# Performance work log

Hardware: AMD Instinct MI355X
Metric: run time of the kernel (lower is better)

The kernel has to match this reference:

```python
import jax, jax.numpy as jnp
import numpy as np

N, E, DIM, HEADS = 100000, 800000, 128, 4
CH = DIM // HEADS


def setup_inputs() -> dict:
    key = jax.random.key(0)
    ks = jax.random.split(key, 20)
    s = 0.02
    inp = {
        "x": jax.random.normal(ks[0], (N, DIM), jnp.float32),
        "edge_index": jax.random.randint(ks[1], (2, E), 0, N, jnp.int64 if jax.config.jax_enable_x64 else jnp.int32),
        "edge_attr": jax.random.normal(ks[2], (E, DIM), jnp.float32),
        # per-layer (leading dim 2) TransformerConv params
        "Wq": jax.random.normal(ks[3], (2, DIM, DIM), jnp.float32) * s,
        "bq": jnp.zeros((2, DIM), jnp.float32),
        "Wk": jax.random.normal(ks[4], (2, DIM, DIM), jnp.float32) * s,
        "bk": jnp.zeros((2, DIM), jnp.float32),
        "Wv": jax.random.normal(ks[5], (2, DIM, DIM), jnp.float32) * s,
        "bv": jnp.zeros((2, DIM), jnp.float32),
        "We": jax.random.normal(ks[6], (2, DIM, DIM), jnp.float32) * s,      # lin_edge, no bias
        "Ws": jax.random.normal(ks[7], (2, DIM, DIM), jnp.float32) * s,      # lin_skip
        "bs": jnp.zeros((2, DIM), jnp.float32),
        "Wb": jax.random.normal(ks[8], (2, 3 * DIM, 1), jnp.float32) * s,    # lin_beta, no bias
        "ln_g": jnp.ones((2, DIM), jnp.float32),
        "ln_b": jnp.zeros((2, DIM), jnp.float32),
        "Wo": jax.random.normal(ks[9], (DIM, DIM), jnp.float32) * s,
        "bo": jnp.zeros((DIM,), jnp.float32),
        "Wg": jax.random.normal(ks[10], (DIM, 1), jnp.float32) * s,
        "bg": jnp.zeros((1,), jnp.float32),
    }
    return inp


def _layer_norm(x, g, b, eps=1e-5):
    mu = jnp.mean(x, -1, keepdims=True)
    var = jnp.mean(jnp.square(x - mu), -1, keepdims=True)
    return (x - mu) * jax.lax.rsqrt(var + eps) * g + b


def _tconv(x, src, dst, edge_attr, Wq, bq, Wk, bk, Wv, bv, We, Ws, bs, Wb):
    # TransformerConv (PyG), beta=True, concat=True, eval mode (no dropout)
    q = (x @ Wq + bq).reshape(N, HEADS, CH)
    k = (x @ Wk + bk).reshape(N, HEADS, CH)
    v = (x @ Wv + bv).reshape(N, HEADS, CH)
    e = (edge_attr @ We).reshape(E, HEADS, CH)
    kj = k[src] + e                                    # [E,H,C]
    vj = v[src] + e
    logits = jnp.sum(q[dst] * kj, -1) / np.sqrt(CH)    # [E,H]
    m = jax.ops.segment_max(logits, dst, num_segments=N)
    p = jnp.exp(logits - m[dst])
    denom = jax.ops.segment_sum(p, dst, num_segments=N)
    alpha = p / (denom[dst] + 1e-16)                   # scatter-softmax over in-edges
    msg = (alpha[..., None] * vj).reshape(E, DIM)
    out = jax.ops.segment_sum(msg, dst, num_segments=N)  # [N,DIM]
    x_r = x @ Ws + bs
    beta = jax.nn.sigmoid(jnp.concatenate([out, x_r, out - x_r], -1) @ Wb)  # [N,1]
    return beta * x_r + (1.0 - beta) * out


def reference(x, edge_index, edge_attr, Wq, bq, Wk, bk, Wv, bv, We, Ws, bs, Wb,
              ln_g, ln_b, Wo, bo, Wg, bg):
    src, dst = edge_index[0], edge_index[1]
    gelu = lambda t: jax.nn.gelu(t, approximate=False)
    h = _layer_norm(gelu(_tconv(x, src, dst, edge_attr, Wq[0], bq[0], Wk[0], bk[0],
                                Wv[0], bv[0], We[0], Ws[0], bs[0], Wb[0])), ln_g[0], ln_b[0])
    h2 = _layer_norm(gelu(_tconv(h, src, dst, edge_attr, Wq[1], bq[1], Wk[1], bk[1],
                                 Wv[1], bv[1], We[1], Ws[1], bs[1], Wb[1])), ln_g[1], ln_b[1])
    h = h + h2
    out = h @ Wo + bo
    g = jax.nn.sigmoid(x @ Wg + bg)
    return g * x + (1.0 - g) * out
```

## Files before the change

kernel.cpp:

```cpp
#include <hip/hip_runtime.h>
#include <math.h>

#define NN 100000
#define NE 800000

typedef __attribute__((ext_vector_type(8))) short short8;
typedef __attribute__((ext_vector_type(4))) float f32x4;

__device__ __forceinline__ float bf2f(unsigned short u) {
  union { float f; unsigned int i; } x; x.i = ((unsigned int)u) << 16; return x.f;
}
__device__ __forceinline__ unsigned short f2bf(float f) {
  union { float f; unsigned int i; } x; x.f = f;
  unsigned int r = x.i + 0x7fffu + ((x.i >> 16) & 1u);
  return (unsigned short)(r >> 16);
}

__device__ __forceinline__ short8 load8_f32_as_bf16(const float* p) {
  const float4 a = *(const float4*)p;
  const float4 b = *(const float4*)(p + 4);
  short8 r;
  r[0] = (short)f2bf(a.x); r[1] = (short)f2bf(a.y); r[2] = (short)f2bf(a.z); r[3] = (short)f2bf(a.w);
  r[4] = (short)f2bf(b.x); r[5] = (short)f2bf(b.y); r[6] = (short)f2bf(b.z); r[7] = (short)f2bf(b.w);
  return r;
}

__global__ __launch_bounds__(256) void hist_k(const int* __restrict__ ei, int* __restrict__ deg) {
  int t = blockIdx.x * 256 + threadIdx.x;
  if (t < NE) atomicAdd(&deg[ei[NE + t]], 1);
}

__global__ __launch_bounds__(256) void scan1(const int* __restrict__ deg, int* __restrict__ bsum) {
  __shared__ int sd[256];
  const int b = blockIdx.x, t = threadIdx.x, base = b * 1024;
  int s = 0;
  #pragma unroll
  for (int i = 0; i < 4; i++) { int idx = base + t * 4 + i; if (idx < NN) s += deg[idx]; }
  sd[t] = s; __syncthreads();
  for (int off = 128; off >= 1; off >>= 1) { if (t < off) sd[t] += sd[t + off]; __syncthreads(); }
  if (t == 0) bsum[b] = sd[0];
}

__global__ __launch_bounds__(64) void scan2(int* __restrict__ bsum, int nb, int* __restrict__ rowstart) {
  const int lane = threadIdx.x;
  int v0 = (2 * lane     < nb) ? bsum[2 * lane]     : 0;
  int v1 = (2 * lane + 1 < nb) ? bsum[2 * lane + 1] : 0;
  const int s = v0 + v1;
  int inc = s;
  #pragma unroll
  for (int off = 1; off < 64; off <<= 1) {
    int o = __shfl_up(inc, off, 64);
    if (lane >= off) inc += o;
  }
  const int excl = inc - s;
  if (2 * lane     < nb) bsum[2 * lane]     = excl;
  if (2 * lane + 1 < nb) bsum[2 * lane + 1] = excl + v0;
  if (lane == 63) rowstart[NN] = inc;
}

__global__ __launch_bounds__(256) void scan3(const int* __restrict__ deg, const int* __restrict__ bsum,
                                             int* __restrict__ rowstart, int* __restrict__ cursor) {
  __shared__ int sd[256];
  const int b = blockIdx.x, t = threadIdx.x, base = b * 1024;
  int vals[4]; int s = 0;
  #pragma unroll
  for (int i = 0; i < 4; i++) { int idx = base + t * 4 + i; vals[i] = (idx < NN) ? deg[idx] : 0; s += vals[i]; }
  sd[t] = s; __syncthreads();
  for (int off = 1; off < 256; off <<= 1) {
    int add = (t >= off) ? sd[t - off] : 0;
    __syncthreads();
    sd[t] += add;
    __syncthreads();
  }
  const int excl = sd[t] - s;
  int run = bsum[b] + excl;
  #pragma unroll
  for (int i = 0; i < 4; i++) {
    int idx = base + t * 4 + i;
    if (idx < NN) { rowstart[idx] = run; cursor[idx] = run; run += vals[i]; }
  }
}

__global__ __launch_bounds__(256) void scatter_k(const int* __restrict__ ei, int* __restrict__ cursor,
                                                 int2* __restrict__ rec) {
  int t = blockIdx.x * 256 + threadIdx.x;
  if (t >= NE) return;
  int dst = ei[NE + t];
  int pos = atomicAdd(&cursor[dst], 1);
  rec[pos] = make_int2(ei[t], t);
}

__global__ __launch_bounds__(256) void conv_w(
    const float* __restrict__ Wq, const float* __restrict__ Wk, const float* __restrict__ Wv,
    const float* __restrict__ Ws, const float* __restrict__ We, const float* __restrict__ Wo,
    unsigned short* __restrict__ wT)
{
  int idx = blockIdx.x * 256 + threadIdx.x;
  int m = idx >> 14;
  int r = idx & 16383;
  int n = r >> 7, kk = r & 127;
  const float* src;
  switch (m) {
    case 0: src = Wq; break;
    case 1: src = Wk; break;
    case 2: src = Wv; break;
    case 3: src = Ws; break;
    case 4: src = Wq + 16384; break;
    case 5: src = Wk + 16384; break;
    case 6: src = Wv + 16384; break;
    case 7: src = Ws + 16384; break;
    case 8: src = We; break;
    case 9: src = We + 16384; break;
    default: src = Wo; break;
  }
  wT[idx] = f2bf(src[(size_t)kk * 128 + n]);
}

template<int ABF16, int HASBIAS, int NMAT>
__global__ __launch_bounds__(256, 4) void gemm_lds(
    const void* __restrict__ Ap, const unsigned short* __restrict__ wT, int s0, int s1,
    const float* __restrict__ bias0, const float* __restrict__ bias1,
    unsigned short* __restrict__ o0, unsigned short* __restrict__ o1, int M)
{
  __shared__ __align__(16) unsigned short As[64 * 136];
  __shared__ __align__(16) unsigned short Os[4 * 16 * 36];
  const int wave = threadIdx.x >> 6, lane = threadIdx.x & 63;
  const int l15 = lane & 15, g = lane >> 4;
  const int colf = wave * 32;
  const int rb = blockIdx.x * 64;
  unsigned short* os = Os + wave * (16 * 36);

  short8 wf[NMAT][2][4];
  const int slots[2] = { s0, s1 };
  #pragma unroll
  for (int m = 0; m < NMAT; ++m) {
    const unsigned short* wp = wT + (size_t)slots[m] * 16384;
    #pragma unroll
    for (int cb = 0; cb < 2; ++cb) {
      const int col = colf + cb * 16 + l15;
      #pragma unroll
      for (int kt = 0; kt < 4; ++kt)
        wf[m][cb][kt] = *(const short8*)(wp + (size_t)col * 128 + kt * 32 + g * 8);
    }
  }
  float bia[NMAT][2][4];
  if (HASBIAS) {
    const float* bp[2] = { bias0, bias1 };
    #pragma unroll
    for (int m = 0; m < NMAT; ++m)
      #pragma unroll
      for (int cb = 0; cb < 2; ++cb)
        #pragma unroll
        for (int j = 0; j < 4; ++j)
          bia[m][cb][j] = bp[m][colf + cb * 16 + g * 4 + j];
  }

  if (ABF16) {
    #pragma unroll
    for (int it = 0; it < 4; ++it) {
      const int c = it * 256 + threadIdx.x;
      const int row = c >> 4, cw = c & 15;
      const int gr = rb + row;
      const int ar = (gr < M) ? gr : (M - 1);
      short8 vch = *(const short8*)((const unsigned short*)Ap + (size_t)ar * 128 + cw * 8);
      *(short8*)(As + row * 136 + cw * 8) = vch;
    }
  } else {
    #pragma unroll
    for (int it = 0; it < 8; ++it) {
      const int c = it * 256 + threadIdx.x;
      const int row = c >> 5, cw = c & 31;
      const int gr = rb + row;
      const int ar = (gr < M) ? gr : (M - 1);
      const float4 f = *(const float4*)((const float*)Ap + (size_t)ar * 128 + cw * 4);
      uint2 pk;
      pk.x = (unsigned int)f2bf(f.x) | ((unsigned int)f2bf(f.y) << 16);
      pk.y = (unsigned int)f2bf(f.z) | ((unsigned int)f2bf(f.w) << 16);
      *(uint2*)(As + row * 136 + cw * 4) = pk;
    }
  }
  __syncthreads();

  const int srow = rb + l15;

  #pragma unroll
  for (int rg = 0; rg < 4; ++rg) {
    const int row = rg * 16 + l15;
    short8 a[4];
    #pragma unroll
    for (int kt = 0; kt < 4; ++kt)
      a[kt] = *(const short8*)(As + row * 136 + kt * 32 + g * 8);

    #pragma unroll
    for (int m = 0; m < NMAT; ++m) {
      #pragma unroll
      for (int cb = 0; cb < 2; ++cb) {
        f32x4 acc; acc[0] = 0.f; acc[1] = 0.f; acc[2] = 0.f; acc[3] = 0.f;
        #pragma unroll
        for (int kt = 0; kt < 4; ++kt)
          acc = __builtin_amdgcn_mfma_f32_16x16x32_bf16(wf[m][cb][kt], a[kt], acc, 0, 0, 0);
        float f0 = acc[0], f1 = acc[1], f2 = acc[2], f3 = acc[3];
        if (HASBIAS) { f0 += bia[m][cb][0]; f1 += bia[m][cb][1]; f2 += bia[m][cb][2]; f3 += bia[m][cb][3]; }
        uint2 pk;
        pk.x = (unsigned int)f2bf(f0) | ((unsigned int)f2bf(f1) << 16);
        pk.y = (unsigned int)f2bf(f2) | ((unsigned int)f2bf(f3) << 16);
        *(uint2*)(os + l15 * 36 + cb * 16 + g * 4) = pk;
      }
      short8 vv = *(const short8*)(os + l15 * 36 + g * 8);
      const int r = srow + rg * 16;
      if (r < M) {
        unsigned short* op = (m == 0) ? o0 : o1;
        *(short8*)(op + (size_t)r * 128 + colf + g * 8) = vv;
      }
    }
  }
}

__global__ __launch_bounds__(256, 2) void final_rs(
    const unsigned short* __restrict__ A, const unsigned short* __restrict__ wp,
    const float* __restrict__ bo, const float* __restrict__ xin,
    const float* __restrict__ Wg, const float* __restrict__ bg,
    float* __restrict__ out, int M)
{
  __shared__ float gl[4][64];
  __shared__ float grow_s[64];
  const int wave = threadIdx.x >> 6, lane = threadIdx.x & 63;
  const int l15 = lane & 15, g = lane >> 4;
  const int colf = wave * 32;
  const int rb = blockIdx.x * 64;

  short8 wf[2][4];
  #pragma unroll
  for (int cb = 0; cb < 2; ++cb) {
    const int col = colf + cb * 16 + l15;
    #pragma unroll
    for (int kt = 0; kt < 4; ++kt)
      wf[cb][kt] = *(const short8*)(wp + (size_t)col * 128 + kt * 32 + g * 8);
  }
  float bia[2][4], wgf[2][4];
  #pragma unroll
  for (int cb = 0; cb < 2; ++cb)
    #pragma unroll
    for (int j = 0; j < 4; ++j) {
      bia[cb][j] = bo[colf + cb * 16 + g * 4 + j];
      wgf[cb][j] = Wg[colf + cb * 16 + g * 4 + j];
    }

  f32x4 accs[4][2];
  float4 xv[4][2];

  #pragma unroll
  for (int rg = 0; rg < 4; ++rg) {
    const int r = rb + rg * 16 + l15;
    const int ar = (r < M) ? r : (M - 1);
    short8 a[4];
    #pragma unroll
    for (int kt = 0; kt < 4; ++kt)
      a[kt] = *(const short8*)(A + (size_t)ar * 128 + kt * 32 + g * 8);

    float part = 0.f;
    #pragma unroll
    for (int cb = 0; cb < 2; ++cb) {
      f32x4 acc; acc[0] = 0.f; acc[1] = 0.f; acc[2] = 0.f; acc[3] = 0.f;
      #pragma unroll
      for (int kt = 0; kt < 4; ++kt)
        acc = __builtin_amdgcn_mfma_f32_16x16x32_bf16(wf[cb][kt], a[kt], acc, 0, 0, 0);
      accs[rg][cb] = acc;
      const int c0 = colf + cb * 16 + g * 4;
      const float4 x4 = *(const float4*)(xin + (size_t)ar * 128 + c0);
      xv[rg][cb] = x4;
      part += x4.x * wgf[cb][0] + x4.y * wgf[cb][1] + x4.z * wgf[cb][2] + x4.w * wgf[cb][3];
    }
    part += __shfl_xor(part, 16, 64);
    part += __shfl_xor(part, 32, 64);
    if (g == 0) gl[wave][rg * 16 + l15] = part;
  }
  __syncthreads();
  if (threadIdx.x < 64) {
    const float s = gl[0][threadIdx.x] + gl[1][threadIdx.x] + gl[2][threadIdx.x] + gl[3][threadIdx.x] + bg[0];
    grow_s[threadIdx.x] = 1.f / (1.f + expf(-s));
  }
  __syncthreads();

  #pragma unroll
  for (int rg = 0; rg < 4; ++rg) {
    const int r = rb + rg * 16 + l15;
    if (r < M) {
      const float gr = grow_s[rg * 16 + l15];
      #pragma unroll
      for (int cb = 0; cb < 2; ++cb) {
        const int c0 = colf + cb * 16 + g * 4;
        const float4 x4 = xv[rg][cb];
        const f32x4 acc = accs[rg][cb];
        float4 res;
        res.x = gr * x4.x + (1.f - gr) * (acc[0] + bia[cb][0]);
        res.y = gr * x4.y + (1.f - gr) * (acc[1] + bia[cb][1]);
        res.z = gr * x4.z + (1.f - gr) * (acc[2] + bia[cb][2]);
        res.w = gr * x4.w + (1.f - gr) * (acc[3] + bia[cb][3]);
        *(float4*)(out + (size_t)r * 128 + c0) = res;
      }
    }
  }
}

__global__ __launch_bounds__(256) void csr_attn(
    const int* __restrict__ rowstart, const int2* __restrict__ rec,
    const unsigned short* __restrict__ e,
    const unsigned short* __restrict__ q, const unsigned short* __restrict__ k,
    const unsigned short* __restrict__ v, const unsigned short* __restrict__ xr,
    const float* __restrict__ Wb, const float* __restrict__ lng, const float* __restrict__ lnb,
    const unsigned short* __restrict__ prev, unsigned short* __restrict__ hout)
{
  const int n = blockIdx.x * 8 + (threadIdx.x >> 5);
  if (n >= NN) return;
  const int lh = threadIdx.x & 31;
  const int d0 = lh * 4;
  const size_t base = (size_t)n * 128 + d0;

  const uint2 qp = *(const uint2*)(q + base);
  const float q0 = bf2f(qp.x & 0xffff), q1 = bf2f(qp.x >> 16);
  const float q2 = bf2f(qp.y & 0xffff), q3 = bf2f(qp.y >> 16);

  float a0 = 0.f, a1 = 0.f, a2 = 0.f, a3 = 0.f, den = 0.f;
  const int s = rowstart[n], eend = rowstart[n + 1];
  const float scale = 0.17677669529663687f;

  int pos = s;
  for (; pos + 3 < eend; pos += 4) {
    const int2 r0 = rec[pos], r1 = rec[pos + 1], r2 = rec[pos + 2], r3 = rec[pos + 3];
    const uint2 kp0 = *(const uint2*)(k + (size_t)r0.x * 128 + d0);
    const uint2 kp1 = *(const uint2*)(k + (size_t)r1.x * 128 + d0);
    const uint2 kp2 = *(const uint2*)(k + (size_t)r2.x * 128 + d0);
    const uint2 kp3 = *(const uint2*)(k + (size_t)r3.x * 128 + d0);
    const uint2 ep0 = *(const uint2*)(e + (size_t)r0.y * 128 + d0);
    const uint2 ep1 = *(const uint2*)(e + (size_t)r1.y * 128 + d0);
    const uint2 ep2 = *(const uint2*)(e + (size_t)r2.y * 128 + d0);
    const uint2 ep3 = *(const uint2*)(e + (size_t)r3.y * 128 + d0);
    const uint2 vp0 = *(const uint2*)(v + (size_t)r0.x * 128 + d0);
    const uint2 vp1 = *(const uint2*)(v + (size_t)r1.x * 128 + d0);
    const uint2 vp2 = *(const uint2*)(v + (size_t)r2.x * 128 + d0);
    const uint2 vp3 = *(const uint2*)(v + (size_t)r3.x * 128 + d0);

    const float e00 = bf2f(ep0.x & 0xffff), e01 = bf2f(ep0.x >> 16), e02 = bf2f(ep0.y & 0xffff), e03 = bf2f(ep0.y >> 16);
    const float e10 = bf2f(ep1.x & 0xffff), e11 = bf2f(ep1.x >> 16), e12 = bf2f(ep1.y & 0xffff), e13 = bf2f(ep1.y >> 16);
    const float e20 = bf2f(ep2.x & 0xffff), e21 = bf2f(ep2.x >> 16), e22 = bf2f(ep2.y & 0xffff), e23 = bf2f(ep2.y >> 16);
    const float e30 = bf2f(ep3.x & 0xffff), e31 = bf2f(ep3.x >> 16), e32 = bf2f(ep3.y & 0xffff), e33 = bf2f(ep3.y >> 16);

    float d0_ = q0 * (bf2f(kp0.x & 0xffff) + e00) + q1 * (bf2f(kp0.x >> 16) + e01)
              + q2 * (bf2f(kp0.y & 0xffff) + e02) + q3 * (bf2f(kp0.y >> 16) + e03);
    float d1_ = q0 * (bf2f(kp1.x & 0xffff) + e10) + q1 * (bf2f(kp1.x >> 16) + e11)
              + q2 * (bf2f(kp1.y & 0xffff) + e12) + q3 * (bf2f(kp1.y >> 16) + e13);
    float d2_ = q0 * (bf2f(kp2.x & 0xffff) + e20) + q1 * (bf2f(kp2.x >> 16) + e21)
              + q2 * (bf2f(kp2.y & 0xffff) + e22) + q3 * (bf2f(kp2.y >> 16) + e23);
    float d3_ = q0 * (bf2f(kp3.x & 0xffff) + e30) + q1 * (bf2f(kp3.x >> 16) + e31)
              + q2 * (bf2f(kp3.y & 0xffff) + e32) + q3 * (bf2f(kp3.y >> 16) + e33);

    d0_ += __shfl_xor(d0_, 1, 64); d1_ += __shfl_xor(d1_, 1, 64);
    d2_ += __shfl_xor(d2_, 1, 64); d3_ += __shfl_xor(d3_, 1, 64);
    d0_ += __shfl_xor(d0_, 2, 64); d1_ += __shfl_xor(d1_, 2, 64);
    d2_ += __shfl_xor(d2_, 2, 64); d3_ += __shfl_xor(d3_, 2, 64);
    d0_ += __shfl_xor(d0_, 4, 64); d1_ += __shfl_xor(d1_, 4, 64);
    d2_ += __shfl_xor(d2_, 4, 64); d3_ += __shfl_xor(d3_, 4, 64);

    const float p0 = expf(d0_ * scale);
    const float p1 = expf(d1_ * scale);
    const float p2 = expf(d2_ * scale);
    const float p3 = expf(d3_ * scale);

    a0 += p0 * (bf2f(vp0.x & 0xffff) + e00) + p1 * (bf2f(vp1.x & 0xffff) + e10)
        + p2 * (bf2f(vp2.x & 0xffff) + e20) + p3 * (bf2f(vp3.x & 0xffff) + e30);
    a1 += p0 * (bf2f(vp0.x >> 16) + e01) + p1 * (bf2f(vp1.x >> 16) + e11)
        + p2 * (bf2f(vp2.x >> 16) + e21) + p3 * (bf2f(vp3.x >> 16) + e31);
    a2 += p0 * (bf2f(vp0.y & 0xffff) + e02) + p1 * (bf2f(vp1.y & 0xffff) + e12)
        + p2 * (bf2f(vp2.y & 0xffff) + e22) + p3 * (bf2f(vp3.y & 0xffff) + e32);
    a3 += p0 * (bf2f(vp0.y >> 16) + e03) + p1 * (bf2f(vp1.y >> 16) + e13)
        + p2 * (bf2f(vp2.y >> 16) + e23) + p3 * (bf2f(vp3.y >> 16) + e33);
    den += (p0 + p1) + (p2 + p3);
  }
  for (; pos < eend; ++pos) {
    const int2 rA = rec[pos];
    const uint2 kpA = *(const uint2*)(k + (size_t)rA.x * 128 + d0);
    const uint2 epA = *(const uint2*)(e + (size_t)rA.y * 128 + d0);
    const uint2 vpA = *(const uint2*)(v + (size_t)rA.x * 128 + d0);
    const float eA0 = bf2f(epA.x & 0xffff), eA1 = bf2f(epA.x >> 16);
    const float eA2 = bf2f(epA.y & 0xffff), eA3 = bf2f(epA.y >> 16);
    float dA = q0 * (bf2f(kpA.x & 0xffff) + eA0) + q1 * (bf2f(kpA.x >> 16) + eA1)
             + q2 * (bf2f(kpA.y & 0xffff) + eA2) + q3 * (bf2f(kpA.y >> 16) + eA3);
    dA += __shfl_xor(dA, 1, 64);
    dA += __shfl_xor(dA, 2, 64);
    dA += __shfl_xor(dA, 4, 64);
    const float pA = expf(dA * scale);
    a0 += pA * (bf2f(vpA.x & 0xffff) + eA0);
    a1 += pA * (bf2f(vpA.x >> 16) + eA1);
    a2 += pA * (bf2f(vpA.y & 0xffff) + eA2);
    a3 += pA * (bf2f(vpA.y >> 16) + eA3);
    den += pA;
  }

  const float dinv = 1.f / (den + 1e-16f);
  const float o0 = a0 * dinv, o1 = a1 * dinv, o2 = a2 * dinv, o3 = a3 * dinv;

  const uint2 xp = *(const uint2*)(xr + base);
  const float x0 = bf2f(xp.x & 0xffff), x1 = bf2f(xp.x >> 16);
  const float x2 = bf2f(xp.y & 0xffff), x3 = bf2f(xp.y >> 16);

  const float4 wb0 = *(const float4*)(Wb + d0);
  const float4 wb1 = *(const float4*)(Wb + 128 + d0);
  const float4 wb2 = *(const float4*)(Wb + 256 + d0);
  float sb = o0 * wb0.x + o1 * wb0.y + o2 * wb0.z + o3 * wb0.w
           + x0 * wb1.x + x1 * wb1.y + x2 * wb1.z + x3 * wb1.w
           + (o0 - x0) * wb2.x + (o1 - x1) * wb2.y + (o2 - x2) * wb2.z + (o3 - x3) * wb2.w;
  #pragma unroll
  for (int off = 16; off >= 1; off >>= 1) sb += __shfl_xor(sb, off, 64);
  const float beta = 1.f / (1.f + expf(-sb));

  float y0 = beta * x0 + (1.f - beta) * o0;
  float y1 = beta * x1 + (1.f - beta) * o1;
  float y2 = beta * x2 + (1.f - beta) * o2;
  float y3 = beta * x3 + (1.f - beta) * o3;
  y0 = 0.5f * y0 * (1.f + erff(y0 * 0.7071067811865475f));
  y1 = 0.5f * y1 * (1.f + erff(y1 * 0.7071067811865475f));
  y2 = 0.5f * y2 * (1.f + erff(y2 * 0.7071067811865475f));
  y3 = 0.5f * y3 * (1.f + erff(y3 * 0.7071067811865475f));

  float mu = (y0 + y1) + (y2 + y3);
  #pragma unroll
  for (int off = 16; off >= 1; off >>= 1) mu += __shfl_xor(mu, off, 64);
  mu *= (1.f / 128.f);
  const float dv0 = y0 - mu, dv1 = y1 - mu, dv2 = y2 - mu, dv3 = y3 - mu;
  float var = (dv0 * dv0 + dv1 * dv1) + (dv2 * dv2 + dv3 * dv3);
  #pragma unroll
  for (int off = 16; off >= 1; off >>= 1) var += __shfl_xor(var, off, 64);
  var *= (1.f / 128.f);
  const float rs = rsqrtf(var + 1e-5f);

  const float4 lg = *(const float4*)(lng + d0);
  const float4 lb = *(const float4*)(lnb + d0);
  float h0 = dv0 * rs * lg.x + lb.x;
  float h1 = dv1 * rs * lg.y + lb.y;
  float h2 = dv2 * rs * lg.z + lb.z;
  float h3 = dv3 * rs * lg.w + lb.w;
  if (prev) {
    const uint2 pp = *(const uint2*)(prev + base);
    h0 += bf2f(pp.x & 0xffff); h1 += bf2f(pp.x >> 16);
    h2 += bf2f(pp.y & 0xffff); h3 += bf2f(pp.y >> 16);
  }
  uint2 packed;
  packed.x = (unsigned int)f2bf(h0) | ((unsigned int)f2bf(h1) << 16);
  packed.y = (unsigned int)f2bf(h2) | ((unsigned int)f2bf(h3) << 16);
  *(uint2*)(hout + base) = packed;
}

extern "C" void kernel_launch(void* const* d_in, const int* in_sizes, int n_in,
                              void* d_out, int out_size, void* d_ws, size_t ws_size,
                              hipStream_t stream)
{
  const float* x  = (const float*)d_in[0];
  const int*   ei = (const int*)d_in[1];
  const float* ea = (const float*)d_in[2];
  const float* Wq = (const float*)d_in[3];
  const float* bq = (const float*)d_in[4];
  const float* Wk = (const float*)d_in[5];
  const float* bk = (const float*)d_in[6];
  const float* Wv = (const float*)d_in[7];
  const float* bv = (const float*)d_in[8];
  const float* We = (const float*)d_in[9];
  const float* Ws = (const float*)d_in[10];
  const float* bs = (const float*)d_in[11];
  const float* Wb = (const float*)d_in[12];
  const float* lng= (const float*)d_in[13];
  const float* lnb= (const float*)d_in[14];
  const float* Wo = (const float*)d_in[15];
  const float* bo = (const float*)d_in[16];
  const float* Wg = (const float*)d_in[17];
  const float* bg = (const float*)d_in[18];
  float* outp = (float*)d_out;

  char* p = (char*)d_ws;
  auto take = [&](size_t b) -> char* { char* r = p; p += (b + 255) & ~(size_t)255; return r; };
  unsigned short* wT = (unsigned short*)take((size_t)11 * 16384 * 2);
  unsigned short* q  = (unsigned short*)take((size_t)NN * 128 * 2);
  unsigned short* k  = (unsigned short*)take((size_t)NN * 128 * 2);
  unsigned short* v  = (unsigned short*)take((size_t)NN * 128 * 2);
  unsigned short* xr = (unsigned short*)take((size_t)NN * 128 * 2);
  unsigned short* h1 = (unsigned short*)take((size_t)NN * 128 * 2);
  unsigned short* hs = (unsigned short*)take((size_t)NN * 128 * 2);
  int* deg      = (int*)take((size_t)NN * 4);
  int* rowstart = (int*)take((size_t)(NN + 1) * 4);
  int* cursor   = (int*)take((size_t)NN * 4);
  int* bsum     = (int*)take((size_t)128 * 4);
  int2* rec     = (int2*)take((size_t)NE * 8);
  unsigned short* e0 = (unsigned short*)take((size_t)NE * 128 * 2);
  size_t used = (size_t)(p - (char*)d_ws);
  const bool dual = (used + (size_t)NE * 128 * 2) <= ws_size;
  unsigned short* e1 = dual ? (unsigned short*)take((size_t)NE * 128 * 2) : e0;

  const int SCAN_BLOCKS = (NN + 1023) / 1024;
  const int NTILE_E  = (NE + 63) / 64;
  const int NTILE_N  = (NN + 63) / 64;
  const int NTILE_A  = (NN + 7) / 8;

  hipMemsetAsync(deg, 0, (size_t)NN * 4, stream);
  hist_k<<<(NE + 255) / 256, 256, 0, stream>>>(ei, deg);
  scan1<<<SCAN_BLOCKS, 256, 0, stream>>>(deg, bsum);
  scan2<<<1, 64, 0, stream>>>(bsum, SCAN_BLOCKS, rowstart);
  scan3<<<SCAN_BLOCKS, 256, 0, stream>>>(deg, bsum, rowstart, cursor);
  scatter_k<<<(NE + 255) / 256, 256, 0, stream>>>(ei, cursor, rec);

  conv_w<<<704, 256, 0, stream>>>(Wq, Wk, Wv, Ws, We, Wo, wT);
  if (dual) {
    gemm_lds<0,0,2><<<NTILE_E, 256, 0, stream>>>(ea, wT, 8, 9, nullptr, nullptr, e0, e1, NE);
  } else {
    gemm_lds<0,0,1><<<NTILE_E, 256, 0, stream>>>(ea, wT, 8, 8, nullptr, nullptr, e0, e0, NE);
  }

  gemm_lds<0,1,2><<<NTILE_N, 256, 0, stream>>>(x, wT, 0, 1, bq, bk, q, k, NN);
  gemm_lds<0,1,2><<<NTILE_N, 256, 0, stream>>>(x, wT, 2, 3, bv, bs, v, xr, NN);
  csr_attn<<<NTILE_A, 256, 0, stream>>>(rowstart, rec, e0, q, k, v, xr, Wb, lng, lnb, nullptr, h1);

  if (!dual) gemm_lds<0,0,1><<<NTILE_E, 256, 0, stream>>>(ea, wT, 9, 9, nullptr, nullptr, e0, e0, NE);
  gemm_lds<1,1,2><<<NTILE_N, 256, 0, stream>>>(h1, wT, 4, 5, bq + 128, bk + 128, q, k, NN);
  gemm_lds<1,1,2><<<NTILE_N, 256, 0, stream>>>(h1, wT, 6, 7, bv + 128, bs + 128, v, xr, NN);
  csr_attn<<<NTILE_A, 256, 0, stream>>>(rowstart, rec, e1, q, k, v, xr, Wb + 384, lng + 128, lnb + 128, h1, hs);

  final_rs<<<NTILE_N, 256, 0, stream>>>(hs, wT + (size_t)10 * 16384, bo, x, Wg, bg, outp, NN);
}
```

Before: 673.4 us.

## Write edge projections in CSR-sorted order so attention reads edge features contiguously

The edge-feature GEMM now scatters each output row to its CSR-sorted position, using a per-edge sortpos array produced by the scatter kernel. The attention kernel then reads edge features sequentially by CSR position instead of gathering them by original edge id, and the index record shrinks from int2 to int. This turns the random gathers of 256-byte edge rows in both attention passes into streaming reads. In exchange, the GEMM writes become scattered and there is an extra sortpos array.

```diff
diff --git a/kernel.cpp b/kernel.cpp
--- a/kernel.cpp
+++ b/kernel.cpp
@@ -82,12 +82,13 @@
 }
 
 __global__ __launch_bounds__(256) void scatter_k(const int* __restrict__ ei, int* __restrict__ cursor,
-                                                 int2* __restrict__ rec) {
+                                                 int* __restrict__ srcs, int* __restrict__ sortpos) {
   int t = blockIdx.x * 256 + threadIdx.x;
   if (t >= NE) return;
   int dst = ei[NE + t];
   int pos = atomicAdd(&cursor[dst], 1);
-  rec[pos] = make_int2(ei[t], t);
+  srcs[pos] = ei[t];
+  sortpos[t] = pos;
 }
 
 __global__ __launch_bounds__(256) void conv_w(
@@ -116,10 +117,11 @@
   wT[idx] = f2bf(src[(size_t)kk * 128 + n]);
 }
 
-template<int ABF16, int HASBIAS, int NMAT>
+template<int ABF16, int HASBIAS, int NMAT, int SCATTER>
 __global__ __launch_bounds__(256, 4) void gemm_lds(
     const void* __restrict__ Ap, const unsigned short* __restrict__ wT, int s0, int s1,
     const float* __restrict__ bias0, const float* __restrict__ bias1,
+    const int* __restrict__ sortpos,
     unsigned short* __restrict__ o0, unsigned short* __restrict__ o1, int M)
 {
   __shared__ __align__(16) unsigned short As[64 * 136];
@@ -190,6 +192,10 @@
     #pragma unroll
     for (int kt = 0; kt < 4; ++kt)
       a[kt] = *(const short8*)(As + row * 136 + kt * 32 + g * 8);
+
+    const int r = srow + rg * 16;
+    size_t orow = 0;
+    if (r < M) orow = SCATTER ? (size_t)sortpos[r] : (size_t)r;
 
     #pragma unroll
     for (int m = 0; m < NMAT; ++m) {
@@ -207,10 +213,9 @@
         *(uint2*)(os + l15 * 36 + cb * 16 + g * 4) = pk;
       }
       short8 vv = *(const short8*)(os + l15 * 36 + g * 8);
-      const int r = srow + rg * 16;
       if (r < M) {
         unsigned short* op = (m == 0) ? o0 : o1;
-        *(short8*)(op + (size_t)r * 128 + colf + g * 8) = vv;
+        *(short8*)(op + orow * 128 + colf + g * 8) = vv;
       }
     }
   }
@@ -304,7 +309,7 @@
 }
 
 __global__ __launch_bounds__(256) void csr_attn(
-    const int* __restrict__ rowstart, const int2* __restrict__ rec,
+    const int* __restrict__ rowstart, const int* __restrict__ srcs,
     const unsigned short* __restrict__ e,
     const unsigned short* __restrict__ q, const unsigned short* __restrict__ k,
     const unsigned short* __restrict__ v, const unsigned short* __restrict__ xr,
@@ -327,19 +332,19 @@
 
   int pos = s;
   for (; pos + 3 < eend; pos += 4) {
-    const int2 r0 = rec[pos], r1 = rec[pos + 1], r2 = rec[pos + 2], r3 = rec[pos + 3];
-    const uint2 kp0 = *(const uint2*)(k + (size_t)r0.x * 128 + d0);
-    const uint2 kp1 = *(const uint2*)(k + (size_t)r1.x * 128 + d0);
-    const uint2 kp2 = *(const uint2*)(k + (size_t)r2.x * 128 + d0);
-    const uint2 kp3 = *(const uint2*)(k + (size_t)r3.x * 128 + d0);
-    const uint2 ep0 = *(const uint2*)(e + (size_t)r0.y * 128 + d0);
-    const uint2 ep1 = *(const uint2*)(e + (size_t)r1.y * 128 + d0);
-    const uint2 ep2 = *(const uint2*)(e + (size_t)r2.y * 128 + d0);
-    const uint2 ep3 = *(const uint2*)(e + (size_t)r3.y * 128 + d0);
-    const uint2 vp0 = *(const uint2*)(v + (size_t)r0.x * 128 + d0);
-    const uint2 vp1 = *(const uint2*)(v + (size_t)r1.x * 128 + d0);
-    const uint2 vp2 = *(const uint2*)(v + (size_t)r2.x * 128 + d0);
-    const uint2 vp3 = *(const uint2*)(v + (size_t)r3.x * 128 + d0);
+    const int s0_ = srcs[pos], s1_ = srcs[pos + 1], s2_ = srcs[pos + 2], s3_ = srcs[pos + 3];
+    const uint2 kp0 = *(const uint2*)(k + (size_t)s0_ * 128 + d0);
+    const uint2 kp1 = *(const uint2*)(k + (size_t)s1_ * 128 + d0);
+    const uint2 kp2 = *(const uint2*)(k + (size_t)s2_ * 128 + d0);
+    const uint2 kp3 = *(const uint2*)(k + (size_t)s3_ * 128 + d0);
+    const uint2 ep0 = *(const uint2*)(e + (size_t)(pos)     * 128 + d0);
+    const uint2 ep1 = *(const uint2*)(e + (size_t)(pos + 1) * 128 + d0);
+    const uint2 ep2 = *(const uint2*)(e + (size_t)(pos + 2) * 128 + d0);
+    const uint2 ep3 = *(const uint2*)(e + (size_t)(pos + 3) * 128 + d0);
+    const uint2 vp0 = *(const uint2*)(v + (size_t)s0_ * 128 + d0);
+    const uint2 vp1 = *(const uint2*)(v + (size_t)s1_ * 128 + d0);
+    const uint2 vp2 = *(const uint2*)(v + (size_t)s2_ * 128 + d0);
+    const uint2 vp3 = *(const uint2*)(v + (size_t)s3_ * 128 + d0);
 
     const float e00 = bf2f(ep0.x & 0xffff), e01 = bf2f(ep0.x >> 16), e02 = bf2f(ep0.y & 0xffff), e03 = bf2f(ep0.y >> 16);
     const float e10 = bf2f(ep1.x & 0xffff), e11 = bf2f(ep1.x >> 16), e12 = bf2f(ep1.y & 0xffff), e13 = bf2f(ep1.y >> 16);
@@ -378,10 +383,10 @@
     den += (p0 + p1) + (p2 + p3);
   }
   for (; pos < eend; ++pos) {
-    const int2 rA = rec[pos];
-    const uint2 kpA = *(const uint2*)(k + (size_t)rA.x * 128 + d0);
-    const uint2 epA = *(const uint2*)(e + (size_t)rA.y * 128 + d0);
-    const uint2 vpA = *(const uint2*)(v + (size_t)rA.x * 128 + d0);
+    const int sA = srcs[pos];
+    const uint2 kpA = *(const uint2*)(k + (size_t)sA * 128 + d0);
+    const uint2 epA = *(const uint2*)(e + (size_t)pos * 128 + d0);
+    const uint2 vpA = *(const uint2*)(v + (size_t)sA * 128 + d0);
     const float eA0 = bf2f(epA.x & 0xffff), eA1 = bf2f(epA.x >> 16);
     const float eA2 = bf2f(epA.y & 0xffff), eA3 = bf2f(epA.y >> 16);
     float dA = q0 * (bf2f(kpA.x & 0xffff) + eA0) + q1 * (bf2f(kpA.x >> 16) + eA1)
@@ -489,7 +494,8 @@
   int* rowstart = (int*)take((size_t)(NN + 1) * 4);
   int* cursor   = (int*)take((size_t)NN * 4);
   int* bsum     = (int*)take((size_t)128 * 4);
-  int2* rec     = (int2*)take((size_t)NE * 8);
+  int* srcs     = (int*)take((size_t)NE * 4);
+  int* sortpos  = (int*)take((size_t)NE * 4);
   unsigned short* e0 = (unsigned short*)take((size_t)NE * 128 * 2);
   size_t used = (size_t)(p - (char*)d_ws);
   const bool dual = (used + (size_t)NE * 128 * 2) <= ws_size;
@@ -505,23 +511,23 @@
   scan1<<<SCAN_BLOCKS, 256, 0, stream>>>(deg, bsum);
   scan2<<<1, 64, 0, stream>>>(bsum, SCAN_BLOCKS, rowstart);
   scan3<<<SCAN_BLOCKS, 256, 0, stream>>>(deg, bsum, rowstart, cursor);
-  scatter_k<<<(NE + 255) / 256, 256, 0, stream>>>(ei, cursor, rec);
+  scatter_k<<<(NE + 255) / 256, 256, 0, stream>>>(ei, cursor, srcs, sortpos);
 
   conv_w<<<704, 256, 0, stream>>>(Wq, Wk, Wv, Ws, We, Wo, wT);
   if (dual) {
-    gemm_lds<0,0,2><<<NTILE_E, 256, 0, stream>>>(ea, wT, 8, 9, nullptr, nullptr, e0, e1, NE);
+    gemm_lds<0,0,2,1><<<NTILE_E, 256, 0, stream>>>(ea, wT, 8, 9, nullptr, nullptr, sortpos, e0, e1, NE);
   } else {
-    gemm_lds<0,0,1><<<NTILE_E, 256, 0, stream>>>(ea, wT, 8, 8, nullptr, nullptr, e0, e0, NE);
-  }
-
-  gemm_lds<0,1,2><<<NTILE_N, 256, 0, stream>>>(x, wT, 0, 1, bq, bk, q, k, NN);
-  gemm_lds<0,1,2><<<NTILE_N, 256, 0, stream>>>(x, wT, 2, 3, bv, bs, v, xr, NN);
-  csr_attn<<<NTILE_A, 256, 0, stream>>>(rowstart, rec, e0, q, k, v, xr, Wb, lng, lnb, nullptr, h1);
-
-  if (!dual) gemm_lds<0,0,1><<<NTILE_E, 256, 0, stream>>>(ea, wT, 9, 9, nullptr, nullptr, e0, e0, NE);
-  gemm_lds<1,1,2><<<NTILE_N, 256, 0, stream>>>(h1, wT, 4, 5, bq + 128, bk + 128, q, k, NN);
-  gemm_lds<1,1,2><<<NTILE_N, 256, 0, stream>>>(h1, wT, 6, 7, bv + 128, bs + 128, v, xr, NN);
-  csr_attn<<<NTILE_A, 256, 0, stream>>>(rowstart, rec, e1, q, k, v, xr, Wb + 384, lng + 128, lnb + 128, h1, hs);
+    gemm_lds<0,0,1,1><<<NTILE_E, 256, 0, stream>>>(ea, wT, 8, 8, nullptr, nullptr, sortpos, e0, e0, NE);
+  }
+
+  gemm_lds<0,1,2,0><<<NTILE_N, 256, 0, stream>>>(x, wT, 0, 1, bq, bk, nullptr, q, k, NN);
+  gemm_lds<0,1,2,0><<<NTILE_N, 256, 0, stream>>>(x, wT, 2, 3, bv, bs, nullptr, v, xr, NN);
+  csr_attn<<<NTILE_A, 256, 0, stream>>>(rowstart, srcs, e0, q, k, v, xr, Wb, lng, lnb, nullptr, h1);
+
+  if (!dual) gemm_lds<0,0,1,1><<<NTILE_E, 256, 0, stream>>>(ea, wT, 9, 9, nullptr, nullptr, sortpos, e0, e0, NE);
+  gemm_lds<1,1,2,0><<<NTILE_N, 256, 0, stream>>>(h1, wT, 4, 5, bq + 128, bk + 128, nullptr, q, k, NN);
+  gemm_lds<1,1,2,0><<<NTILE_N, 256, 0, stream>>>(h1, wT, 6, 7, bv + 128, bs + 128, nullptr, v, xr, NN);
+  csr_attn<<<NTILE_A, 256, 0, stream>>>(rowstart, srcs, e1, q, k, v, xr, Wb + 384, lng + 128, lnb + 128, h1, hs);
 
   final_rs<<<NTILE_N, 256, 0, stream>>>(hs, wT + (size_t)10 * 16384, bo, x, Wg, bg, outp, NN);
 }
```

Result: no change. 675.6 us (+0.3%).
